# Optimization experiments

Measured on AMD Instinct MI355X. Metric: run time of the kernel, lower is better.

The kernel has to match this reference:

```python
import jax, jax.numpy as jnp
import numpy as np

B, NQ, NK, QS, KS, H, VD = 16, 64, 512, 256, 256, 256, 256


def setup_inputs() -> dict:
    key = jax.random.key(0)
    k1, k2, k3, k4, k5, k6, k7 = jax.random.split(key, 7)
    return {
        "queries": jax.random.normal(k1, (B, NQ, QS), dtype=jnp.float32),
        "keys": jax.random.normal(k2, (B, NK, KS), dtype=jnp.float32),
        "values": jax.random.normal(k3, (B, NK, VD), dtype=jnp.float32),
        "valid_lens": jax.random.randint(k4, (B,), 1, NK + 1, dtype=jnp.int32),
        # learned params (nn.Linear with bias=False): W_q [QS,H], W_k [KS,H], w_v [H]
        "W_q": jax.random.normal(k5, (QS, H), dtype=jnp.float32) / np.sqrt(QS),
        "W_k": jax.random.normal(k6, (KS, H), dtype=jnp.float32) / np.sqrt(KS),
        "w_v": jax.random.normal(k7, (H,), dtype=jnp.float32) / np.sqrt(H),
    }


def reference(queries, keys, values, valid_lens, W_q, W_k, w_v):
    # project: q [B,nq,H], k [B,nk,H]
    q = jnp.einsum("bqd,dh->bqh", queries, W_q)
    k = jnp.einsum("bkd,dh->bkh", keys, W_k)
    # broadcast-add -> tanh -> score reduction via w_v: [B,nq,nk]
    features = jnp.tanh(q[:, :, None, :] + k[:, None, :, :])  # [B,nq,nk,H]
    scores = jnp.einsum("bqkh,h->bqk", features, w_v)
    # masked softmax over keys (positions >= valid_len masked out)
    mask = jnp.arange(scores.shape[-1])[None, None, :] < valid_lens[:, None, None]
    scores = jnp.where(mask, scores, -1e6)
    attn = jax.nn.softmax(scores, axis=-1)
    # weighted sum of values (dropout p=0 / eval mode => identity)
    return jnp.einsum("bqk,bkv->bqv", attn, values)
```

## Files before the change

kernel.cpp:

```cpp
#include <hip/hip_runtime.h>
#include <hip/hip_bf16.h>

#define BB 16
#define NQ 64
#define NK 512
#define HD 256

typedef __attribute__((ext_vector_type(8))) short short8;
typedef __attribute__((ext_vector_type(4))) float f32x4;

__device__ inline ushort bf16_rne(float v) {
    unsigned u = __float_as_uint(v);
    return (ushort)((u + 0x7FFFu + ((u >> 16) & 1u)) >> 16);
}
__device__ inline float bf16_to_f(ushort h) {
    return __uint_as_float(((unsigned)h) << 16);
}

__global__ __launch_bounds__(256, 2) void proj_mfma(
    const float* __restrict__ queries, const float* __restrict__ keys,
    const float* __restrict__ W_q, const float* __restrict__ W_k,
    float* __restrict__ qp, float* __restrict__ kp, float scale)
{
    __shared__ ushort AsH[128][72];
    __shared__ ushort AsL[128][72];
    __shared__ ushort WtH[64][72];
    __shared__ ushort WtL[64][72];

    const float* A; const float* W; float* C; int rows0;
    const int rb = blockIdx.x;
    if (rb < 8) { A = queries; W = W_q; C = qp; rows0 = rb * 128; }
    else        { A = keys;    W = W_k; C = kp; rows0 = (rb - 8) * 128; }
    const int cols0 = blockIdx.y * 64;

    const int t    = threadIdx.x;
    const int lane = t & 63;
    const int wave = t >> 6;
    const int quad = lane >> 4;
    const int l15  = lane & 15;

    f32x4 acc[2][4];
    #pragma unroll
    for (int i = 0; i < 2; ++i)
        #pragma unroll
        for (int j = 0; j < 4; ++j)
            acc[i][j] = (f32x4){0.f, 0.f, 0.f, 0.f};

    for (int k0 = 0; k0 < 256; k0 += 64) {
        float4 av[8];
        #pragma unroll
        for (int i = 0; i < 8; ++i) {
            int idx = i * 256 + t;
            int row = idx >> 4, kf = (idx & 15) * 4;
            av[i] = *(const float4*)&A[(size_t)(rows0 + row) * 256 + k0 + kf];
        }
        float4 wv[4];
        #pragma unroll
        for (int i = 0; i < 4; ++i) {
            int idx = i * 256 + t;
            int krow = idx >> 4, nf = (idx & 15) * 4;
            wv[i] = *(const float4*)&W[(size_t)(k0 + krow) * 256 + cols0 + nf];
        }
        __syncthreads();

        #pragma unroll
        for (int i = 0; i < 8; ++i) {
            int idx = i * 256 + t;
            int row = idx >> 4, kf = (idx & 15) * 4;
            float fv[4] = {av[i].x, av[i].y, av[i].z, av[i].w};
            ushort hh[4], ll[4];
            #pragma unroll
            for (int c = 0; c < 4; ++c) {
                hh[c] = bf16_rne(fv[c]);
                ll[c] = bf16_rne(fv[c] - bf16_to_f(hh[c]));
            }
            *(ushort4*)&AsH[row][kf] = make_ushort4(hh[0], hh[1], hh[2], hh[3]);
            *(ushort4*)&AsL[row][kf] = make_ushort4(ll[0], ll[1], ll[2], ll[3]);
        }
        #pragma unroll
        for (int i = 0; i < 4; ++i) {
            int idx = i * 256 + t;
            int krow = idx >> 4, nf = (idx & 15) * 4;
            float fv[4] = {wv[i].x, wv[i].y, wv[i].z, wv[i].w};
            #pragma unroll
            for (int c = 0; c < 4; ++c) {
                ushort hh = bf16_rne(fv[c]);
                WtH[nf + c][krow] = hh;
                WtL[nf + c][krow] = bf16_rne(fv[c] - bf16_to_f(hh));
            }
        }
        __syncthreads();

        #pragma unroll
        for (int ks = 0; ks < 64; ks += 32) {
            short8 aH[2], aL[2], bH[4], bL[4];
            #pragma unroll
            for (int ms = 0; ms < 2; ++ms) {
                int r = wave * 32 + ms * 16 + l15;
                aH[ms] = *(const short8*)&AsH[r][ks + quad * 8];
                aL[ms] = *(const short8*)&AsL[r][ks + quad * 8];
            }
            #pragma unroll
            for (int ns = 0; ns < 4; ++ns) {
                int n = ns * 16 + l15;
                bH[ns] = *(const short8*)&WtH[n][ks + quad * 8];
                bL[ns] = *(const short8*)&WtL[n][ks + quad * 8];
            }
            #pragma unroll
            for (int ms = 0; ms < 2; ++ms)
                #pragma unroll
                for (int ns = 0; ns < 4; ++ns) {
                    acc[ms][ns] = __builtin_amdgcn_mfma_f32_16x16x32_bf16(aH[ms], bH[ns], acc[ms][ns], 0, 0, 0);
                    acc[ms][ns] = __builtin_amdgcn_mfma_f32_16x16x32_bf16(aL[ms], bH[ns], acc[ms][ns], 0, 0, 0);
                    acc[ms][ns] = __builtin_amdgcn_mfma_f32_16x16x32_bf16(aH[ms], bL[ns], acc[ms][ns], 0, 0, 0);
                }
        }
    }

    #pragma unroll
    for (int ms = 0; ms < 2; ++ms) {
        int rbase = rows0 + wave * 32 + ms * 16 + quad * 4;
        #pragma unroll
        for (int ns = 0; ns < 4; ++ns) {
            int col = cols0 + ns * 16 + l15;
            #pragma unroll
            for (int r = 0; r < 4; ++r)
                C[(size_t)(rbase + r) * 256 + col] = acc[ms][ns][r] * scale;
        }
    }
}

__global__ __launch_bounds__(256, 2) void attn_kernel(
    const float* __restrict__ qp,
    const float* __restrict__ kp,
    const float* __restrict__ values,
    const int*   __restrict__ vlens,
    const float* __restrict__ w_v,
    float* __restrict__ out)
{
    __shared__ float q_s[2][HD];
    __shared__ float wv_s[HD];
    __shared__ float sc[2][NK];
    __shared__ float part[4][2][HD];
    __shared__ float redm[4], reds[4], invs[2];

    const int b     = blockIdx.x & 15;
    const int qpair = blockIdx.x >> 4;
    const int qi0   = qpair * 2;
    const int t     = threadIdx.x;
    const int lane  = t & 63;
    const int wave  = t >> 6;
    const int vl    = vlens[b];
    const size_t row0 = (size_t)b * NQ + qi0;

    q_s[0][t] = qp[row0 * HD + t];
    q_s[1][t] = qp[(row0 + 1) * HD + t];
    wv_s[t]   = w_v[t];
    __syncthreads();

    float Wsum;
    {
        float ws = wv_s[lane] + wv_s[lane + 64] + wv_s[lane + 128] + wv_s[lane + 192];
        #pragma unroll
        for (int off = 32; off; off >>= 1) ws += __shfl_xor(ws, off);
        Wsum = ws;
    }

    const float* kbase = kp + (size_t)b * NK * HD;
    const int nLoc = lane >> 2;
    const int ch   = lane & 3;

    for (int nBase = wave * 16; nBase < vl; nBase += 64) {
        const int n = nBase + nLoc;
        float p0 = 0.f, p1 = 0.f;
        if (n < vl) {
            const float* krow = kbase + (size_t)n * HD + ch * 4;
            float4 kk[16];
            #pragma unroll
            for (int j = 0; j < 16; ++j) kk[j] = *(const float4*)&krow[j * 16];
            #pragma unroll
            for (int j = 0; j < 16; ++j) {
                const int ho = ch * 4 + j * 16;
                float4 k4 = kk[j];
                float4 w4 = *(const float4*)&wv_s[ho];
                float4 qa = *(const float4*)&q_s[0][ho];
                float4 qb = *(const float4*)&q_s[1][ho];

                float r0 = __builtin_amdgcn_rcpf(__builtin_amdgcn_exp2f(qa.x + k4.x) + 1.f);
                float r1 = __builtin_amdgcn_rcpf(__builtin_amdgcn_exp2f(qa.y + k4.y) + 1.f);
                float r2 = __builtin_amdgcn_rcpf(__builtin_amdgcn_exp2f(qa.z + k4.z) + 1.f);
                float r3 = __builtin_amdgcn_rcpf(__builtin_amdgcn_exp2f(qa.w + k4.w) + 1.f);
                p0 = fmaf(w4.x, r0, p0);
                p0 = fmaf(w4.y, r1, p0);
                p0 = fmaf(w4.z, r2, p0);
                p0 = fmaf(w4.w, r3, p0);

                float s0 = __builtin_amdgcn_rcpf(__builtin_amdgcn_exp2f(qb.x + k4.x) + 1.f);
                float s1 = __builtin_amdgcn_rcpf(__builtin_amdgcn_exp2f(qb.y + k4.y) + 1.f);
                float s2 = __builtin_amdgcn_rcpf(__builtin_amdgcn_exp2f(qb.z + k4.z) + 1.f);
                float s3 = __builtin_amdgcn_rcpf(__builtin_amdgcn_exp2f(qb.w + k4.w) + 1.f);
                p1 = fmaf(w4.x, s0, p1);
                p1 = fmaf(w4.y, s1, p1);
                p1 = fmaf(w4.z, s2, p1);
                p1 = fmaf(w4.w, s3, p1);
            }
        }
        p0 += __shfl_down(p0, 2); p0 += __shfl_down(p0, 1);
        p1 += __shfl_down(p1, 2); p1 += __shfl_down(p1, 1);
        if (ch == 0 && n < vl) {
            sc[0][n] = fmaf(-2.f, p0, Wsum);
            sc[1][n] = fmaf(-2.f, p1, Wsum);
        }
    }
    __syncthreads();

    const int vla = (vl + 15) & ~15;
    {
        const int qq  = wave >> 1;
        const int sub = wave & 1;
        float m = -1e30f;
        for (int n = sub * 64 + lane; n < vl; n += 128) m = fmaxf(m, sc[qq][n]);
        #pragma unroll
        for (int off = 32; off; off >>= 1) m = fmaxf(m, __shfl_xor(m, off));
        if (lane == 0) redm[wave] = m;
        __syncthreads();
        m = fmaxf(redm[qq * 2], redm[qq * 2 + 1]);

        float ssum = 0.f;
        const float L2E = 1.4426950408889634f;
        for (int n = sub * 64 + lane; n < vl; n += 128) {
            float p = __builtin_amdgcn_exp2f((sc[qq][n] - m) * L2E);
            sc[qq][n] = p;
            ssum += p;
        }
        #pragma unroll
        for (int off = 32; off; off >>= 1) ssum += __shfl_xor(ssum, off);
        if (lane == 0) reds[wave] = ssum;
        if (vl + t < vla) { sc[0][vl + t] = 0.f; sc[1][vl + t] = 0.f; }
        __syncthreads();
        if (t == 0)  invs[0] = __builtin_amdgcn_rcpf(reds[0] + reds[1]);
        if (t == 64) invs[1] = __builtin_amdgcn_rcpf(reds[2] + reds[3]);
    }
    __syncthreads();

    float4 acc0 = {0.f, 0.f, 0.f, 0.f};
    float4 acc1 = {0.f, 0.f, 0.f, 0.f};
    const float* vbase = values + (size_t)b * NK * HD;
    for (int nb = wave * 4; nb < vla; nb += 16) {
        float4 v[4]; float pa[4], pb[4];
        #pragma unroll
        for (int u = 0; u < 4; ++u) {
            v[u]  = *(const float4*)&vbase[(size_t)(nb + u) * HD + lane * 4];
            pa[u] = sc[0][nb + u];
            pb[u] = sc[1][nb + u];
        }
        #pragma unroll
        for (int u = 0; u < 4; ++u) {
            acc0.x = fmaf(pa[u], v[u].x, acc0.x);
            acc0.y = fmaf(pa[u], v[u].y, acc0.y);
            acc0.z = fmaf(pa[u], v[u].z, acc0.z);
            acc0.w = fmaf(pa[u], v[u].w, acc0.w);
            acc1.x = fmaf(pb[u], v[u].x, acc1.x);
            acc1.y = fmaf(pb[u], v[u].y, acc1.y);
            acc1.z = fmaf(pb[u], v[u].z, acc1.z);
            acc1.w = fmaf(pb[u], v[u].w, acc1.w);
        }
    }
    *(float4*)&part[wave][0][lane * 4] = acc0;
    *(float4*)&part[wave][1][lane * 4] = acc1;
    __syncthreads();

    if (wave < 2) {
        float4 p0 = *(const float4*)&part[0][wave][lane * 4];
        float4 p1 = *(const float4*)&part[1][wave][lane * 4];
        float4 p2 = *(const float4*)&part[2][wave][lane * 4];
        float4 p3 = *(const float4*)&part[3][wave][lane * 4];
        const float inv = invs[wave];
        float4 o;
        o.x = ((p0.x + p1.x) + (p2.x + p3.x)) * inv;
        o.y = ((p0.y + p1.y) + (p2.y + p3.y)) * inv;
        o.z = ((p0.z + p1.z) + (p2.z + p3.z)) * inv;
        o.w = ((p0.w + p1.w) + (p2.w + p3.w)) * inv;
        *(float4*)&out[(row0 + wave) * HD + lane * 4] = o;
    }
}

extern "C" void kernel_launch(void* const* d_in, const int* in_sizes, int n_in,
                              void* d_out, int out_size, void* d_ws, size_t ws_size,
                              hipStream_t stream) {
    const float* queries = (const float*)d_in[0];
    const float* keys    = (const float*)d_in[1];
    const float* values  = (const float*)d_in[2];
    const int*   vlens   = (const int*)d_in[3];
    const float* W_q     = (const float*)d_in[4];
    const float* W_k     = (const float*)d_in[5];
    const float* w_v     = (const float*)d_in[6];
    float* out = (float*)d_out;

    float* kp = (float*)d_ws;
    float* qp = out;

    const float SC = 2.885390081777927f;

    proj_mfma<<<dim3(72, 4), 256, 0, stream>>>(queries, keys, W_q, W_k, qp, kp, SC);
    attn_kernel<<<dim3(512), 256, 0, stream>>>(qp, kp, values, vlens, w_v, out);
}
```

Baseline: 122.6 us.

## Pre-split inputs to bf16 hi/lo in separate pass, swizzle LDS, register-cache q in attention

```diff
diff --git a/kernel.cpp b/kernel.cpp
--- a/kernel.cpp
+++ b/kernel.cpp
@@ -9,35 +9,77 @@
 typedef __attribute__((ext_vector_type(8))) short short8;
 typedef __attribute__((ext_vector_type(4))) float f32x4;
 
-__device__ inline ushort bf16_rne(float v) {
+__device__ __forceinline__ ushort bf16_rne(float v) {
     unsigned u = __float_as_uint(v);
     return (ushort)((u + 0x7FFFu + ((u >> 16) & 1u)) >> 16);
 }
-__device__ inline float bf16_to_f(ushort h) {
+__device__ __forceinline__ float bf16_to_f(ushort h) {
     return __uint_as_float(((unsigned)h) << 16);
 }
 
-__global__ __launch_bounds__(256, 2) void proj_mfma(
-    const float* __restrict__ queries, const float* __restrict__ keys,
-    const float* __restrict__ W_q, const float* __restrict__ W_k,
+__global__ __launch_bounds__(256) void convert_split(
+    const float* __restrict__ q, const float* __restrict__ k,
+    const float* __restrict__ wq, const float* __restrict__ wk,
+    ushort* __restrict__ qh, ushort* __restrict__ ql,
+    ushort* __restrict__ kh, ushort* __restrict__ kl,
+    ushort* __restrict__ wqh, ushort* __restrict__ wql,
+    ushort* __restrict__ wkh, ushort* __restrict__ wkl)
+{
+    const int idx = blockIdx.x * 256 + threadIdx.x;
+    if (blockIdx.x < 2304) {
+        int e = idx * 4;
+        const float* src; ushort *dh, *dl; int off;
+        if (e < 1024 * 256) { src = q; dh = qh; dl = ql; off = e; }
+        else { src = k; dh = kh; dl = kl; off = e - 1024 * 256; }
+        float4 v = *(const float4*)&src[off];
+        float fv[4] = {v.x, v.y, v.z, v.w};
+        ushort hh[4], ll[4];
+        #pragma unroll
+        for (int c = 0; c < 4; ++c) {
+            hh[c] = bf16_rne(fv[c]);
+            ll[c] = bf16_rne(fv[c] - bf16_to_f(hh[c]));
+        }
+        *(ushort4*)&dh[off] = make_ushort4(hh[0], hh[1], hh[2], hh[3]);
+        *(ushort4*)&dl[off] = make_ushort4(ll[0], ll[1], ll[2], ll[3]);
+    } else {
+        int widx = idx - 2304 * 256;
+        const float* W; ushort *wh, *wl;
+        if (widx < 16384) { W = wq; wh = wqh; wl = wql; }
+        else { W = wk; wh = wkh; wl = wkl; widx -= 16384; }
+        int kk = widx >> 6;
+        int n4 = (widx & 63) * 4;
+        float4 v = *(const float4*)&W[kk * 256 + n4];
+        float fv[4] = {v.x, v.y, v.z, v.w};
+        #pragma unroll
+        for (int c = 0; c < 4; ++c) {
+            ushort hh = bf16_rne(fv[c]);
+            wh[(n4 + c) * 256 + kk] = hh;
+            wl[(n4 + c) * 256 + kk] = bf16_rne(fv[c] - bf16_to_f(hh));
+        }
+    }
+}
+
+__global__ __launch_bounds__(256, 2) void proj_mfma2(
+    const ushort* __restrict__ qh, const ushort* __restrict__ ql,
+    const ushort* __restrict__ kh, const ushort* __restrict__ kl,
+    const ushort* __restrict__ wqh, const ushort* __restrict__ wql,
+    const ushort* __restrict__ wkh, const ushort* __restrict__ wkl,
     float* __restrict__ qp, float* __restrict__ kp, float scale)
 {
-    __shared__ ushort AsH[128][72];
-    __shared__ ushort AsL[128][72];
-    __shared__ ushort WtH[64][72];
-    __shared__ ushort WtL[64][72];
-
-    const float* A; const float* W; float* C; int rows0;
-    const int rb = blockIdx.x;
-    if (rb < 8) { A = queries; W = W_q; C = qp; rows0 = rb * 128; }
-    else        { A = keys;    W = W_k; C = kp; rows0 = (rb - 8) * 128; }
+    __shared__ ushort AsH[128 * 64], AsL[128 * 64];
+    __shared__ ushort BsH[64 * 64],  BsL[64 * 64];
+
+    const ushort *Ah, *Al, *Bh, *Bl; float* C; int rows0;
+    if (blockIdx.x < 8) { Ah = qh; Al = ql; Bh = wqh; Bl = wql; C = qp; rows0 = blockIdx.x * 128; }
+    else                { Ah = kh; Al = kl; Bh = wkh; Bl = wkl; C = kp; rows0 = (blockIdx.x - 8) * 128; }
     const int cols0 = blockIdx.y * 64;
 
-    const int t    = threadIdx.x;
-    const int lane = t & 63;
-    const int wave = t >> 6;
-    const int quad = lane >> 4;
-    const int l15  = lane & 15;
+    const int t = threadIdx.x, lane = t & 63, wave = t >> 6;
+    const int quad = lane >> 4, l15 = lane & 15;
+    const int lr = lane >> 3;
+    const int cg = (lane & 7) ^ lr;
+    const int swz0 = quad ^ (l15 & 7);
+    const int swz1 = (quad + 4) ^ (l15 & 7);
 
     f32x4 acc[2][4];
     #pragma unroll
@@ -47,64 +89,52 @@
             acc[i][j] = (f32x4){0.f, 0.f, 0.f, 0.f};
 
     for (int k0 = 0; k0 < 256; k0 += 64) {
-        float4 av[8];
-        #pragma unroll
-        for (int i = 0; i < 8; ++i) {
-            int idx = i * 256 + t;
-            int row = idx >> 4, kf = (idx & 15) * 4;
-            av[i] = *(const float4*)&A[(size_t)(rows0 + row) * 256 + k0 + kf];
-        }
-        float4 wv[4];
+        short8 rAh[4], rAl[4], rBh[2], rBl[2];
         #pragma unroll
         for (int i = 0; i < 4; ++i) {
-            int idx = i * 256 + t;
-            int krow = idx >> 4, nf = (idx & 15) * 4;
-            wv[i] = *(const float4*)&W[(size_t)(k0 + krow) * 256 + cols0 + nf];
+            int ii = wave * 4 + i;
+            size_t g = (size_t)(rows0 + ii * 8 + lr) * 256 + k0 + cg * 8;
+            rAh[i] = *(const short8*)&Ah[g];
+            rAl[i] = *(const short8*)&Al[g];
+        }
+        #pragma unroll
+        for (int j = 0; j < 2; ++j) {
+            int jj = wave * 2 + j;
+            size_t g = (size_t)(cols0 + jj * 8 + lr) * 256 + k0 + cg * 8;
+            rBh[j] = *(const short8*)&Bh[g];
+            rBl[j] = *(const short8*)&Bl[g];
         }
         __syncthreads();
 
         #pragma unroll
-        for (int i = 0; i < 8; ++i) {
-            int idx = i * 256 + t;
-            int row = idx >> 4, kf = (idx & 15) * 4;
-            float fv[4] = {av[i].x, av[i].y, av[i].z, av[i].w};
-            ushort hh[4], ll[4];
-            #pragma unroll
-            for (int c = 0; c < 4; ++c) {
-                hh[c] = bf16_rne(fv[c]);
-                ll[c] = bf16_rne(fv[c] - bf16_to_f(hh[c]));
-            }
-            *(ushort4*)&AsH[row][kf] = make_ushort4(hh[0], hh[1], hh[2], hh[3]);
-            *(ushort4*)&AsL[row][kf] = make_ushort4(ll[0], ll[1], ll[2], ll[3]);
-        }
-        #pragma unroll
         for (int i = 0; i < 4; ++i) {
-            int idx = i * 256 + t;
-            int krow = idx >> 4, nf = (idx & 15) * 4;
-            float fv[4] = {wv[i].x, wv[i].y, wv[i].z, wv[i].w};
-            #pragma unroll
-            for (int c = 0; c < 4; ++c) {
-                ushort hh = bf16_rne(fv[c]);
-                WtH[nf + c][krow] = hh;
-                WtL[nf + c][krow] = bf16_rne(fv[c] - bf16_to_f(hh));
-            }
+            int ci = (wave * 4 + i) * 64 + lane;
+            *(short8*)&AsH[ci * 8] = rAh[i];
+            *(short8*)&AsL[ci * 8] = rAl[i];
+        }
+        #pragma unroll
+        for (int j = 0; j < 2; ++j) {
+            int ci = (wave * 2 + j) * 64 + lane;
+            *(short8*)&BsH[ci * 8] = rBh[j];
+            *(short8*)&BsL[ci * 8] = rBl[j];
         }
         __syncthreads();
 
         #pragma unroll
-        for (int ks = 0; ks < 64; ks += 32) {
+        for (int ks = 0; ks < 2; ++ks) {
+            const int s = ks ? swz1 : swz0;
             short8 aH[2], aL[2], bH[4], bL[4];
             #pragma unroll
             for (int ms = 0; ms < 2; ++ms) {
                 int r = wave * 32 + ms * 16 + l15;
-                aH[ms] = *(const short8*)&AsH[r][ks + quad * 8];
-                aL[ms] = *(const short8*)&AsL[r][ks + quad * 8];
+                aH[ms] = *(const short8*)&AsH[r * 64 + s * 8];
+                aL[ms] = *(const short8*)&AsL[r * 64 + s * 8];
             }
             #pragma unroll
             for (int ns = 0; ns < 4; ++ns) {
                 int n = ns * 16 + l15;
-                bH[ns] = *(const short8*)&WtH[n][ks + quad * 8];
-                bL[ns] = *(const short8*)&WtL[n][ks + quad * 8];
+                bH[ns] = *(const short8*)&BsH[n * 64 + s * 8];
+                bL[ns] = *(const short8*)&BsL[n * 64 + s * 8];
             }
             #pragma unroll
             for (int ms = 0; ms < 2; ++ms)
@@ -166,51 +196,61 @@
         Wsum = ws;
     }
 
+    const int keyLoc = lane >> 4;
+    const int ch     = lane & 15;
+    float4 qa[4], qb[4], wf[4];
+    #pragma unroll
+    for (int m = 0; m < 4; ++m) {
+        qa[m] = *(const float4*)&q_s[0][ch * 4 + m * 64];
+        qb[m] = *(const float4*)&q_s[1][ch * 4 + m * 64];
+        wf[m] = *(const float4*)&wv_s[ch * 4 + m * 64];
+    }
+
     const float* kbase = kp + (size_t)b * NK * HD;
-    const int nLoc = lane >> 2;
-    const int ch   = lane & 3;
-
-    for (int nBase = wave * 16; nBase < vl; nBase += 64) {
-        const int n = nBase + nLoc;
+    const int n0 = wave * 4 + keyLoc;
+    const float* kptr = kbase + (size_t)n0 * HD + ch * 4;
+
+    float4 kk[4];
+    if (n0 < vl) {
+        #pragma unroll
+        for (int m = 0; m < 4; ++m) kk[m] = *(const float4*)(kptr + m * 64);
+    }
+
+    for (int nBase = wave * 4; nBase < vl; nBase += 16) {
+        const int nn = nBase + keyLoc;
+        float4 kn[4];
+        if (nn + 16 < vl) {
+            #pragma unroll
+            for (int m = 0; m < 4; ++m) kn[m] = *(const float4*)(kptr + 16 * HD + m * 64);
+        }
         float p0 = 0.f, p1 = 0.f;
-        if (n < vl) {
-            const float* krow = kbase + (size_t)n * HD + ch * 4;
-            float4 kk[16];
-            #pragma unroll
-            for (int j = 0; j < 16; ++j) kk[j] = *(const float4*)&krow[j * 16];
-            #pragma unroll
-            for (int j = 0; j < 16; ++j) {
-                const int ho = ch * 4 + j * 16;
-                float4 k4 = kk[j];
-                float4 w4 = *(const float4*)&wv_s[ho];
-                float4 qa = *(const float4*)&q_s[0][ho];
-                float4 qb = *(const float4*)&q_s[1][ho];
-
-                float r0 = __builtin_amdgcn_rcpf(__builtin_amdgcn_exp2f(qa.x + k4.x) + 1.f);
-                float r1 = __builtin_amdgcn_rcpf(__builtin_amdgcn_exp2f(qa.y + k4.y) + 1.f);
-                float r2 = __builtin_amdgcn_rcpf(__builtin_amdgcn_exp2f(qa.z + k4.z) + 1.f);
-                float r3 = __builtin_amdgcn_rcpf(__builtin_amdgcn_exp2f(qa.w + k4.w) + 1.f);
-                p0 = fmaf(w4.x, r0, p0);
-                p0 = fmaf(w4.y, r1, p0);
-                p0 = fmaf(w4.z, r2, p0);
-                p0 = fmaf(w4.w, r3, p0);
-
-                float s0 = __builtin_amdgcn_rcpf(__builtin_amdgcn_exp2f(qb.x + k4.x) + 1.f);
-                float s1 = __builtin_amdgcn_rcpf(__builtin_amdgcn_exp2f(qb.y + k4.y) + 1.f);
-                float s2 = __builtin_amdgcn_rcpf(__builtin_amdgcn_exp2f(qb.z + k4.z) + 1.f);
-                float s3 = __builtin_amdgcn_rcpf(__builtin_amdgcn_exp2f(qb.w + k4.w) + 1.f);
-                p1 = fmaf(w4.x, s0, p1);
-                p1 = fmaf(w4.y, s1, p1);
-                p1 = fmaf(w4.z, s2, p1);
-                p1 = fmaf(w4.w, s3, p1);
+        if (nn < vl) {
+            #pragma unroll
+            for (int m = 0; m < 4; ++m) {
+                float kv[4] = {kk[m].x, kk[m].y, kk[m].z, kk[m].w};
+                float qav[4] = {qa[m].x, qa[m].y, qa[m].z, qa[m].w};
+                float qbv[4] = {qb[m].x, qb[m].y, qb[m].z, qb[m].w};
+                float wv4[4] = {wf[m].x, wf[m].y, wf[m].z, wf[m].w};
+                #pragma unroll
+                for (int c = 0; c < 4; ++c) {
+                    float r0 = __builtin_amdgcn_rcpf(__builtin_amdgcn_exp2f(qav[c] + kv[c]) + 1.f);
+                    float r1 = __builtin_amdgcn_rcpf(__builtin_amdgcn_exp2f(qbv[c] + kv[c]) + 1.f);
+                    p0 = fmaf(wv4[c], r0, p0);
+                    p1 = fmaf(wv4[c], r1, p1);
+                }
             }
         }
+        p0 += __shfl_down(p0, 8); p0 += __shfl_down(p0, 4);
         p0 += __shfl_down(p0, 2); p0 += __shfl_down(p0, 1);
+        p1 += __shfl_down(p1, 8); p1 += __shfl_down(p1, 4);
         p1 += __shfl_down(p1, 2); p1 += __shfl_down(p1, 1);
-        if (ch == 0 && n < vl) {
-            sc[0][n] = fmaf(-2.f, p0, Wsum);
-            sc[1][n] = fmaf(-2.f, p1, Wsum);
-        }
+        if (ch == 0 && nn < vl) {
+            sc[0][nn] = fmaf(-2.f, p0, Wsum);
+            sc[1][nn] = fmaf(-2.f, p1, Wsum);
+        }
+        #pragma unroll
+        for (int m = 0; m < 4; ++m) kk[m] = kn[m];
+        kptr += 16 * HD;
     }
     __syncthreads();
 
@@ -297,11 +337,25 @@
     const float* w_v     = (const float*)d_in[6];
     float* out = (float*)d_out;
 
-    float* kp = (float*)d_ws;
+    float*  kp  = (float*)d_ws;
+    ushort* qh  = (ushort*)((char*)d_ws + (8 << 20));
+    ushort* ql  = qh  + 1024 * 256;
+    ushort* kh  = ql  + 1024 * 256;
+    ushort* kl  = kh  + 8192 * 256;
+    ushort* wqh = kl  + 8192 * 256;
+    ushort* wql = wqh + 65536;
+    ushort* wkh = wql + 65536;
+    ushort* wkl = wkh + 65536;
+
     float* qp = out;
 
     const float SC = 2.885390081777927f;
 
-    proj_mfma<<<dim3(72, 4), 256, 0, stream>>>(queries, keys, W_q, W_k, qp, kp, SC);
+    convert_split<<<dim3(2432), 256, 0, stream>>>(queries, keys, W_q, W_k,
+                                                  qh, ql, kh, kl,
+                                                  wqh, wql, wkh, wkl);
+    proj_mfma2<<<dim3(72, 4), 256, 0, stream>>>(qh, ql, kh, kl,
+                                                wqh, wql, wkh, wkl,
+                                                qp, kp, SC);
     attn_kernel<<<dim3(512), 256, 0, stream>>>(qp, kp, values, vlens, w_v, out);
 }
```

After: 123.5 us. About the same (+0.8%).
